# Kernel tuning notes

Measured on AMD Instinct MI355X. Metric: run time of the kernel, lower is better.

Reference implementation:

```python
import jax, jax.numpy as jnp
import numpy as np

B, H, W = 8, 256, 256
ALPHA = 1.0
BETA = 1.0
EPS = 1e-06
_INF = 1e10  # stands in for +inf in fp32 min-plus EDT


def _minplus_1d(f):
    """Exact 1D squared-distance transform along the last axis.
    g[..., i] = min_j ( f[..., j] + (i - j)^2 )."""
    n = f.shape[-1]
    i = jnp.arange(n)
    D = ((i[:, None] - i[None, :]) ** 2).astype(f.dtype)  # [n, n]
    # broadcast: [..., 1, n] + [n, n] -> [..., n, n] -> min over j
    return jnp.min(f[..., None, :] + D, axis=-1)


def _edt(binary):
    """Exact Euclidean distance to the nearest zero element of `binary`
    (matches scipy.ndimage.distance_transform_edt). binary: [..., H, W]."""
    f = jnp.where(binary > 0.5, _INF, 0.0)
    g = _minplus_1d(f)                         # pass along W
    h = _minplus_1d(jnp.swapaxes(g, -1, -2))   # pass along H
    return jnp.sqrt(jnp.swapaxes(h, -1, -2))


def setup_inputs() -> dict:
    key = jax.random.key(0)
    k1, k2 = jax.random.split(key)
    pred = jax.random.normal(k1, (B, 1, H, W), dtype=jnp.float32)
    target = jax.random.randint(k2, (B, 1, H, W), 0, 2).astype(jnp.float32)
    return {"pred": pred, "target": target, "from_logits": 1}


def reference(pred, target, from_logits):
    if from_logits:
        pred = jax.nn.sigmoid(pred)
    # dice loss
    intersection = 2.0 * jnp.sum(pred * target, axis=(1, 2, 3))
    union = jnp.sum(pred ** 2, axis=(1, 2, 3)) + jnp.sum(target ** 2, axis=(1, 2, 3))
    d_loss = jnp.mean(1.0 - (intersection + EPS) / (union + EPS))
    # boundary loss: dist_out (EDT of ~mask) + dist_in (EDT of mask), no grad
    t = jax.lax.stop_gradient(target[:, 0])  # [B, H, W]
    dist_map = _edt(1.0 - t) + _edt(t)        # [B, H, W]
    b_loss = jnp.mean(pred * dist_map[:, None, :, :])
    return ALPHA * d_loss + BETA * b_loss
```

## Files before the change

### kernel.cpp

```cpp
#include <hip/hip_runtime.h>
#include <math.h>

#define BB 8
#define HH 256
#define WW 256
#define SW 8
#define NBLK (BB*32)
#define NT 512
#define EPSF 1e-6f
#define MSTRIDE 68
#define GSTRIDE 20

__device__ __forceinline__ int nearest_dist(const unsigned long long* m, int c)
{
    const int w = c >> 6, o = c & 63;
    int dr = 256;
    const unsigned long long right = m[w] >> o;
    if (right) dr = __builtin_ctzll(right);
    else {
        for (int ww = w + 1; ww < 4; ++ww)
            if (m[ww]) { dr = (ww - w) * 64 - o + __builtin_ctzll(m[ww]); break; }
    }
    int dl = 256;
    const unsigned long long left = m[w] << (63 - o);
    if (left) dl = __builtin_clzll(left);
    else {
        for (int ww = w - 1; ww >= 0; --ww)
            if (m[ww]) { dl = o + 1 + (w - ww - 1) * 64 + __builtin_clzll(m[ww]); break; }
    }
    const int n = dr < dl ? dr : dl;
    return n < 255 ? n : 255;
}

__global__ __launch_bounds__(NT) void k_fused(
    const float* __restrict__ pred, const float* __restrict__ target,
    const int* __restrict__ from_logits, float* __restrict__ part)
{
    __shared__ unsigned char maskb[HH * MSTRIDE];
    __shared__ unsigned char gbuf[HH * GSTRIDE];
    __shared__ float red[32];

    const int blk = blockIdx.x;
    const int b   = blk >> 5;
    const int c0  = (blk & 31) * SW;
    const int t   = threadIdx.x;
    const int fl  = *from_logits;
    const float* tb = target + b * HH * WW;
    const float* pb = pred   + b * HH * WW;

    {
        const float4* t4 = (const float4*)tb;
        #pragma unroll 4
        for (int i = 0; i < 32; ++i) {
            const int f = i * NT + t;
            const float4 v = t4[f];
            const int row = f >> 6;
            const int q   = f & 63;
            const unsigned nib = (v.x > 0.5f ? 1u : 0u) | (v.y > 0.5f ? 2u : 0u)
                               | (v.z > 0.5f ? 4u : 0u) | (v.w > 0.5f ? 8u : 0u);
            maskb[row * MSTRIDE + q] = (unsigned char)nib;
        }
    }
    __syncthreads();

    {
        const int row = t >> 1;
        const int k0  = (t & 1) * 4;
        const unsigned char* mb = maskb + row * MSTRIDE;
        unsigned long long m[4];
        #pragma unroll
        for (int w = 0; w < 4; ++w) {
            unsigned long long acc = 0ull;
            #pragma unroll
            for (int j = 0; j < 4; ++j) {
                unsigned x = *(const unsigned*)(mb + (w * 4 + j) * 4);
                x = (x | (x >> 4)) & 0x00FF00FFu;
                x = (x | (x >> 8)) & 0x0000FFFFu;
                acc |= ((unsigned long long)x) << (16 * j);
            }
            m[w] = acc;
        }
        const unsigned long long mi[4] = { ~m[0], ~m[1], ~m[2], ~m[3] };
        unsigned lo = 0, hi = 0;
        #pragma unroll
        for (int j = 0; j < 4; ++j) {
            const int c  = c0 + k0 + j;
            const unsigned n1 = (unsigned)nearest_dist(m,  c);
            const unsigned n0 = (unsigned)nearest_dist(mi, c);
            const unsigned pv = n1 | (n0 << 8);
            if (j < 2) lo |= pv << (16 * j);
            else       hi |= pv << (16 * (j - 2));
        }
        *(unsigned*)(gbuf + row * GSTRIDE + k0 * 2)     = lo;
        *(unsigned*)(gbuf + row * GSTRIDE + k0 * 2 + 4) = hi;
    }
    __syncthreads();

    float s_pt = 0.0f, s_p2 = 0.0f, s_st = 0.0f, s_bd = 0.0f;
    {
        const int k  = t & 7;
        const int c  = c0 + k;
        const int r0 = (t >> 3) * 4;
        float pv[4];
        #pragma unroll
        for (int rr = 0; rr < 4; ++rr) pv[rr] = pb[(r0 + rr) * WW + c];

        #pragma unroll 2
        for (int rr = 0; rr < 4; ++rr) {
            const int r = r0 + rr;
            const float p  = pv[rr];
            const float sp = fl ? (1.0f / (1.0f + __expf(-p))) : p;
            const unsigned short vc = *(const unsigned short*)(gbuf + r * GSTRIDE + 2 * k);
            const int n1 = vc & 255, n0 = vc >> 8;
            int best1 = n1 * n1, best0 = n0 * n0;
            for (int d = 1;; ++d) {
                const int dd = d * d;
                if (dd >= best1 && dd >= best0) break;
                const int u = r - d, v2 = r + d;
                if (u >= 0) {
                    const unsigned short vu = *(const unsigned short*)(gbuf + u * GSTRIDE + 2 * k);
                    const int a = vu & 255, bq = vu >> 8;
                    best1 = min(best1, a * a + dd);
                    best0 = min(best0, bq * bq + dd);
                }
                if (v2 < HH) {
                    const unsigned short vd = *(const unsigned short*)(gbuf + v2 * GSTRIDE + 2 * k);
                    const int a = vd & 255, bq = vd >> 8;
                    best1 = min(best1, a * a + dd);
                    best0 = min(best0, bq * bq + dd);
                }
            }
            const float dist = sqrtf((float)best1) + sqrtf((float)best0);
            const int bit = (maskb[r * MSTRIDE + (c >> 2)] >> (c & 3)) & 1;
            const float tv = (float)bit;
            s_pt += sp * tv;
            s_p2 += sp * sp;
            s_st += tv;
            s_bd += sp * dist;
        }
    }

    #pragma unroll
    for (int o = 32; o > 0; o >>= 1) {
        s_pt += __shfl_down(s_pt, o);
        s_p2 += __shfl_down(s_p2, o);
        s_st += __shfl_down(s_st, o);
        s_bd += __shfl_down(s_bd, o);
    }
    const int lane = t & 63, wid = t >> 6;
    if (lane == 0) {
        red[wid] = s_pt; red[8 + wid] = s_p2;
        red[16 + wid] = s_st; red[24 + wid] = s_bd;
    }
    __syncthreads();
    if (t == 0) {
        float a = 0, b2 = 0, cc = 0, dd = 0;
        #pragma unroll
        for (int w = 0; w < 8; ++w) {
            a  += red[w];      b2 += red[8 + w];
            cc += red[16 + w]; dd += red[24 + w];
        }
        part[blk * 4 + 0] = a;  part[blk * 4 + 1] = b2;
        part[blk * 4 + 2] = cc; part[blk * 4 + 3] = dd;
    }
}

__global__ __launch_bounds__(64) void k_final(
    const float* __restrict__ part, float* __restrict__ out)
{
    const int t = threadIdx.x;
    const int b = t >> 3, j = t & 7;
    float pt = 0, p2 = 0, st = 0, bd = 0;
    #pragma unroll
    for (int s = j; s < 32; s += 8) {
        const int idx = (b * 32 + s) * 4;
        pt += part[idx + 0]; p2 += part[idx + 1];
        st += part[idx + 2]; bd += part[idx + 3];
    }
    #pragma unroll
    for (int o = 4; o > 0; o >>= 1) {
        pt += __shfl_down(pt, o, 8);
        p2 += __shfl_down(p2, o, 8);
        st += __shfl_down(st, o, 8);
        bd += __shfl_down(bd, o, 8);
    }
    float dice = (j == 0) ? (1.0f - (2.0f * pt + EPSF) / (p2 + st + EPSF)) : 0.0f;
    float bdv  = (j == 0) ? bd : 0.0f;
    #pragma unroll
    for (int o = 8; o < 64; o <<= 1) {
        dice += __shfl_down(dice, o);
        bdv  += __shfl_down(bdv, o);
    }
    if (t == 0)
        out[0] = dice / (float)BB + bdv / (float)(BB * HH * WW);
}

extern "C" void kernel_launch(void* const* d_in, const int* in_sizes, int n_in,
                              void* d_out, int out_size, void* d_ws, size_t ws_size,
                              hipStream_t stream) {
    const float* pred   = (const float*)d_in[0];
    const float* target = (const float*)d_in[1];
    const int*   fl     = (const int*)d_in[2];
    float* out  = (float*)d_out;
    float* part = (float*)d_ws;

    k_fused<<<NBLK, NT, 0, stream>>>(pred, target, fl, part);
    k_final<<<1, 64, 0, stream>>>(part, out);
}
```

Measured before the change: 70.04 us.

## Process four columns per thread in column pass with vectorized loads and batch-interleaved blocks

The vertical EDT pass now gives each thread one row and four adjacent columns instead of four rows and one column. Pred is loaded as a float4 and the nearest-distance pairs as a uint2 from a 24-byte-stride buffer, so the outward search loop is shared across four columns. Block indexing now interleaves batches (b = blk & 7), and the final reduction indexing is updated to match. The cost is that the shared search runs until the slowest of the eight distances converges, which may add iterations and increase per-thread register use.

Measured after the change: 67.52 us. -3.6%, faster.

```diff
diff --git a/kernel.cpp b/kernel.cpp
--- a/kernel.cpp
+++ b/kernel.cpp
@@ -9,7 +9,7 @@
 #define NT 512
 #define EPSF 1e-6f
 #define MSTRIDE 68
-#define GSTRIDE 20
+#define GSTRIDE 24
 
 __device__ __forceinline__ int nearest_dist(const unsigned long long* m, int c)
 {
@@ -36,13 +36,13 @@
     const float* __restrict__ pred, const float* __restrict__ target,
     const int* __restrict__ from_logits, float* __restrict__ part)
 {
-    __shared__ unsigned char maskb[HH * MSTRIDE];
-    __shared__ unsigned char gbuf[HH * GSTRIDE];
+    __shared__ __align__(16) unsigned char maskb[HH * MSTRIDE];
+    __shared__ __align__(16) unsigned char gbuf[HH * GSTRIDE];
     __shared__ float red[32];
 
     const int blk = blockIdx.x;
-    const int b   = blk >> 5;
-    const int c0  = (blk & 31) * SW;
+    const int b   = blk & 7;
+    const int c0  = (blk >> 3) * SW;
     const int t   = threadIdx.x;
     const int fl  = *from_logits;
     const float* tb = target + b * HH * WW;
@@ -98,45 +98,69 @@
 
     float s_pt = 0.0f, s_p2 = 0.0f, s_st = 0.0f, s_bd = 0.0f;
     {
-        const int k  = t & 7;
-        const int c  = c0 + k;
-        const int r0 = (t >> 3) * 4;
-        float pv[4];
-        #pragma unroll
-        for (int rr = 0; rr < 4; ++rr) pv[rr] = pb[(r0 + rr) * WW + c];
-
-        #pragma unroll 2
-        for (int rr = 0; rr < 4; ++rr) {
-            const int r = r0 + rr;
-            const float p  = pv[rr];
-            const float sp = fl ? (1.0f / (1.0f + __expf(-p))) : p;
-            const unsigned short vc = *(const unsigned short*)(gbuf + r * GSTRIDE + 2 * k);
-            const int n1 = vc & 255, n0 = vc >> 8;
-            int best1 = n1 * n1, best0 = n0 * n0;
-            for (int d = 1;; ++d) {
-                const int dd = d * d;
-                if (dd >= best1 && dd >= best0) break;
-                const int u = r - d, v2 = r + d;
-                if (u >= 0) {
-                    const unsigned short vu = *(const unsigned short*)(gbuf + u * GSTRIDE + 2 * k);
-                    const int a = vu & 255, bq = vu >> 8;
-                    best1 = min(best1, a * a + dd);
-                    best0 = min(best0, bq * bq + dd);
-                }
-                if (v2 < HH) {
-                    const unsigned short vd = *(const unsigned short*)(gbuf + v2 * GSTRIDE + 2 * k);
-                    const int a = vd & 255, bq = vd >> 8;
-                    best1 = min(best1, a * a + dd);
-                    best0 = min(best0, bq * bq + dd);
-                }
+        const int r = t >> 1;
+        const int q = t & 1;
+        const float4 p4 = *(const float4*)&pb[r * WW + c0 + 4 * q];
+        float sp[4];
+        sp[0] = fl ? (1.0f / (1.0f + __expf(-p4.x))) : p4.x;
+        sp[1] = fl ? (1.0f / (1.0f + __expf(-p4.y))) : p4.y;
+        sp[2] = fl ? (1.0f / (1.0f + __expf(-p4.z))) : p4.z;
+        sp[3] = fl ? (1.0f / (1.0f + __expf(-p4.w))) : p4.w;
+
+        const uint2 vc = *(const uint2*)(gbuf + r * GSTRIDE + 8 * q);
+        int b1[4], b0[4];
+        {
+            const unsigned w0 = vc.x, w1 = vc.y;
+            const int n10 = w0 & 255,        n00 = (w0 >> 8) & 255;
+            const int n11 = (w0 >> 16) & 255, n01 = (w0 >> 24) & 255;
+            const int n12 = w1 & 255,        n02 = (w1 >> 8) & 255;
+            const int n13 = (w1 >> 16) & 255, n03 = (w1 >> 24) & 255;
+            b1[0] = n10 * n10; b0[0] = n00 * n00;
+            b1[1] = n11 * n11; b0[1] = n01 * n01;
+            b1[2] = n12 * n12; b0[2] = n02 * n02;
+            b1[3] = n13 * n13; b0[3] = n03 * n03;
+        }
+        for (int d = 1;; ++d) {
+            const int dd = d * d;
+            int mx = b1[0];
+            #pragma unroll
+            for (int j = 0; j < 4; ++j) { mx = max(mx, b1[j]); mx = max(mx, b0[j]); }
+            if (dd >= mx) break;
+            const int u = r - d, v2 = r + d;
+            if (u >= 0) {
+                const uint2 vu = *(const uint2*)(gbuf + u * GSTRIDE + 8 * q);
+                const unsigned w0 = vu.x, w1 = vu.y;
+                const int a0 = w0 & 255, c0b = (w0 >> 8) & 255;
+                const int a1 = (w0 >> 16) & 255, c1b = (w0 >> 24) & 255;
+                const int a2 = w1 & 255, c2b = (w1 >> 8) & 255;
+                const int a3 = (w1 >> 16) & 255, c3b = (w1 >> 24) & 255;
+                b1[0] = min(b1[0], a0 * a0 + dd); b0[0] = min(b0[0], c0b * c0b + dd);
+                b1[1] = min(b1[1], a1 * a1 + dd); b0[1] = min(b0[1], c1b * c1b + dd);
+                b1[2] = min(b1[2], a2 * a2 + dd); b0[2] = min(b0[2], c2b * c2b + dd);
+                b1[3] = min(b1[3], a3 * a3 + dd); b0[3] = min(b0[3], c3b * c3b + dd);
             }
-            const float dist = sqrtf((float)best1) + sqrtf((float)best0);
-            const int bit = (maskb[r * MSTRIDE + (c >> 2)] >> (c & 3)) & 1;
-            const float tv = (float)bit;
-            s_pt += sp * tv;
-            s_p2 += sp * sp;
+            if (v2 < HH) {
+                const uint2 vd = *(const uint2*)(gbuf + v2 * GSTRIDE + 8 * q);
+                const unsigned w0 = vd.x, w1 = vd.y;
+                const int a0 = w0 & 255, c0b = (w0 >> 8) & 255;
+                const int a1 = (w0 >> 16) & 255, c1b = (w0 >> 24) & 255;
+                const int a2 = w1 & 255, c2b = (w1 >> 8) & 255;
+                const int a3 = (w1 >> 16) & 255, c3b = (w1 >> 24) & 255;
+                b1[0] = min(b1[0], a0 * a0 + dd); b0[0] = min(b0[0], c0b * c0b + dd);
+                b1[1] = min(b1[1], a1 * a1 + dd); b0[1] = min(b0[1], c1b * c1b + dd);
+                b1[2] = min(b1[2], a2 * a2 + dd); b0[2] = min(b0[2], c2b * c2b + dd);
+                b1[3] = min(b1[3], a3 * a3 + dd); b0[3] = min(b0[3], c3b * c3b + dd);
+            }
+        }
+        const unsigned nib = maskb[r * MSTRIDE + (c0 >> 2) + q];
+        #pragma unroll
+        for (int j = 0; j < 4; ++j) {
+            const float dist = sqrtf((float)b1[j]) + sqrtf((float)b0[j]);
+            const float tv = (float)((nib >> j) & 1);
+            s_pt += sp[j] * tv;
+            s_p2 += sp[j] * sp[j];
             s_st += tv;
-            s_bd += sp * dist;
+            s_bd += sp[j] * dist;
         }
     }
 
@@ -173,7 +197,7 @@
     float pt = 0, p2 = 0, st = 0, bd = 0;
     #pragma unroll
     for (int s = j; s < 32; s += 8) {
-        const int idx = (b * 32 + s) * 4;
+        const int idx = (b + 8 * s) * 4;
         pt += part[idx + 0]; p2 += part[idx + 1];
         st += part[idx + 2]; bd += part[idx + 3];
     }
```
